# Performance work log

Measured on AMD Instinct MI355X. Metric: run time of the kernel, lower is better.

The kernel has to match this reference:

```python
import jax, jax.numpy as jnp
import numpy as np
import math

B, S, H = 8, 160, 768
DEP = 64
NH, DH = 12, H // 12
W_EDGE = 1.0
EPS = 1e-5


def setup_inputs() -> dict:
    key = jax.random.key(0)
    ks = jax.random.split(key, 16)
    sc_h = 1.0 / math.sqrt(H)
    sc_d = 1.0 / math.sqrt(DEP)
    return {
        "token_feature": jax.random.normal(ks[0], (B, S, H), jnp.float32),
        "edge_feature": jax.random.normal(ks[1], (B, S, S, DEP), jnp.float32),
        "dependency_masks": jax.random.randint(ks[2], (B, S, S), 0, 2, jnp.int32),
        "Wq": jax.random.normal(ks[3], (H, H), jnp.float32) * sc_h,
        "bq": jnp.zeros((H,), jnp.float32),
        "Wk": jax.random.normal(ks[4], (H, H), jnp.float32) * sc_h,
        "bk": jnp.zeros((H,), jnp.float32),
        "Wv": jax.random.normal(ks[5], (H, H), jnp.float32) * sc_h,
        "bv": jnp.zeros((H,), jnp.float32),
        "Wek": jax.random.normal(ks[6], (DEP, H), jnp.float32) * sc_d,
        "bek": jnp.zeros((H,), jnp.float32),
        "Wev": jax.random.normal(ks[7], (DEP, H), jnp.float32) * sc_d,
        "bev": jnp.zeros((H,), jnp.float32),
        "ln_g": jnp.ones((H,), jnp.float32),
        "ln_b": jnp.zeros((H,), jnp.float32),
    }


def _heads3(x):  # [B,S,H] -> [B,NH,S,DH]
    return x.reshape(B, S, NH, DH).transpose(0, 2, 1, 3)


def _heads4(x):  # [B,S,S,H] -> [B,NH,S,S,DH]
    return x.reshape(B, S, S, NH, DH).transpose(0, 3, 1, 2, 4)


def reference(token_feature, edge_feature, dependency_masks,
              Wq, bq, Wk, bk, Wv, bv, Wek, bek, Wev, bev, ln_g, ln_b):
    q = _heads3(token_feature @ Wq + bq)   # [B,NH,S,DH]
    k = _heads3(token_feature @ Wk + bk)
    v = _heads3(token_feature @ Wv + bv)
    ek = _heads4(edge_feature @ Wek + bek)  # [B,NH,S,S,DH]
    ev = _heads4(edge_feature @ Wev + bev)
    # key_ij = k_j + w*ek_ij ; scores_ij = q_i . key_ij / sqrt(dh)
    scores = (jnp.einsum('bhid,bhjd->bhij', q, k)
              + W_EDGE * jnp.einsum('bhid,bhijd->bhij', q, ek))
    scores = scores / math.sqrt(DH)
    mask = (dependency_masks[:, None, :, :] == 0)  # [B,1,S,S]
    scores = jnp.where(mask, jnp.float32(-10000.0), scores)
    probs = jax.nn.softmax(scores, axis=-1)  # dropout is identity in eval
    ctx = (jnp.einsum('bhij,bhjd->bhid', probs, v)
           + W_EDGE * jnp.einsum('bhij,bhijd->bhid', probs, ev))
    ctx = ctx.transpose(0, 2, 1, 3).reshape(B, S, H)
    x = token_feature + ctx
    mu = jnp.mean(x, axis=-1, keepdims=True)
    var = jnp.mean(jnp.square(x - mu), axis=-1, keepdims=True)
    return (x - mu) / jnp.sqrt(var + EPS) * ln_g + ln_b
```

## Files before the change

### kernel.cpp

```cpp
#include <hip/hip_runtime.h>
#include <hip/hip_bf16.h>
#include <math.h>

#define BB 8
#define SS 160
#define HH 768
#define DEPTH 64
#define NHEAD 12
#define DHEAD 64
#define BS (BB*SS)

constexpr float EPS_C = 1e-5f;

typedef __attribute__((ext_vector_type(8))) short bf16x8;
typedef __attribute__((ext_vector_type(4))) float f32x4;

__device__ inline short f2bs(float x) {
    union { __hip_bfloat16 b; short s; } u;
    u.b = __float2bfloat16(x);
    return u.s;
}

__global__ __launch_bounds__(256) void cast_x(
    const float* __restrict__ X, __hip_bfloat16* __restrict__ Xb)
{
    int idx = blockIdx.x * 256 + threadIdx.x;
    float4 xin = ((const float4*)X)[idx];
    __hip_bfloat16* o = Xb + (size_t)idx * 4;
    o[0] = __float2bfloat16(xin.x); o[1] = __float2bfloat16(xin.y);
    o[2] = __float2bfloat16(xin.z); o[3] = __float2bfloat16(xin.w);
}

__global__ __launch_bounds__(256) void transpose_cast_w(
    const float* __restrict__ Wq, const float* __restrict__ Wk,
    const float* __restrict__ Wv, __hip_bfloat16* __restrict__ WT)
{
    __shared__ float t[32][33];
    const float* W = (blockIdx.z == 0) ? Wq : (blockIdx.z == 1) ? Wk : Wv;
    __hip_bfloat16* o = WT + (size_t)blockIdx.z * HH * HH;
    int kt = blockIdx.x * 32, nt = blockIdx.y * 32;
    int tx = threadIdx.x & 31, ty = threadIdx.x >> 5;
#pragma unroll
    for (int r = 0; r < 32; r += 8)
        t[ty + r][tx] = W[(size_t)(kt + ty + r) * HH + nt + tx];
    __syncthreads();
#pragma unroll
    for (int r = 0; r < 32; r += 8)
        o[(size_t)(nt + ty + r) * HH + kt + tx] = __float2bfloat16(t[tx][ty + r]);
}

__global__ __launch_bounds__(256) void gemm_qkv(
    const __hip_bfloat16* __restrict__ Xb, const __hip_bfloat16* __restrict__ WT,
    const float* __restrict__ bq, const float* __restrict__ bk,
    const float* __restrict__ bv,
    __hip_bfloat16* __restrict__ qb, __hip_bfloat16* __restrict__ kb,
    __hip_bfloat16* __restrict__ vb)
{
    __shared__ int4 sA[4][128];
    __shared__ int4 sB[4][64];
    int m0 = blockIdx.x * 128, n0 = blockIdx.y * 64, mat = blockIdx.z;
    const short* X = (const short*)Xb;
    const short* W = (const short*)WT + (size_t)mat * HH * HH;
    const float* bias = (mat == 0) ? bq : (mat == 1) ? bk : bv;
    int tid = threadIdx.x, w = tid >> 6, l = tid & 63;
    int wm = (w >> 1) * 64, wn = (w & 1) * 32;
    int khalf = l >> 4, lc = l & 15;

    f32x4 acc[4][2];
#pragma unroll
    for (int i = 0; i < 4; i++)
#pragma unroll
        for (int j = 0; j < 2; j++) acc[i][j] = (f32x4){0.f, 0.f, 0.f, 0.f};

    for (int k0 = 0; k0 < HH; k0 += 32) {
        __syncthreads();
        sA[w][l]      = *(const int4*)(X + (size_t)(m0 + l) * HH + k0 + w * 8);
        sA[w][l + 64] = *(const int4*)(X + (size_t)(m0 + l + 64) * HH + k0 + w * 8);
        sB[w][l]      = *(const int4*)(W + (size_t)(n0 + l) * HH + k0 + w * 8);
        __syncthreads();
        bf16x8 b0 = *(const bf16x8*)&sB[khalf][wn + lc];
        bf16x8 b1 = *(const bf16x8*)&sB[khalf][wn + 16 + lc];
#pragma unroll
        for (int mi = 0; mi < 4; mi++) {
            bf16x8 a = *(const bf16x8*)&sA[khalf][wm + mi * 16 + lc];
            acc[mi][0] = __builtin_amdgcn_mfma_f32_16x16x32_bf16(a, b0, acc[mi][0], 0, 0, 0);
            acc[mi][1] = __builtin_amdgcn_mfma_f32_16x16x32_bf16(a, b1, acc[mi][1], 0, 0, 0);
        }
    }

    int rg = (l >> 4) * 4;
    __hip_bfloat16* outm = (mat == 0) ? qb : (mat == 1) ? kb : vb;
#pragma unroll
    for (int ni = 0; ni < 2; ni++) {
        int gcol = n0 + wn + ni * 16 + lc;
        float bv_ = bias[gcol];
#pragma unroll
        for (int mi = 0; mi < 4; mi++) {
            int grow = m0 + wm + mi * 16 + rg;
            f32x4 a = acc[mi][ni];
            __hip_bfloat16* o = outm + (size_t)grow * HH + gcol;
            o[0]      = __float2bfloat16(a.x + bv_);
            o[HH]     = __float2bfloat16(a.y + bv_);
            o[2 * HH] = __float2bfloat16(a.z + bv_);
            o[3 * HH] = __float2bfloat16(a.w + bv_);
        }
    }
}

__global__ __launch_bounds__(256) void scores_gemm(
    const __hip_bfloat16* __restrict__ qb, const __hip_bfloat16* __restrict__ kb,
    _Float16* __restrict__ sc)
{
    __shared__ int4 sQ[8][160];
    __shared__ int4 sK[8][160];
    int h = blockIdx.x, b = blockIdx.y;
    const short* Q = (const short*)qb + (size_t)b * SS * HH + h * DHEAD;
    const short* K = (const short*)kb + (size_t)b * SS * HH + h * DHEAD;
    int tid = threadIdx.x, w = tid >> 6, l = tid & 63;

    for (int idx = tid; idx < SS * 8; idx += 256) {
        int row = idx >> 3, ch = idx & 7;
        sQ[ch][row] = *(const int4*)(Q + (size_t)row * HH + ch * 8);
        sK[ch][row] = *(const int4*)(K + (size_t)row * HH + ch * 8);
    }
    __syncthreads();

    int wm = (w >> 1) * 80, wn = (w & 1) * 80;
    int khalf = l >> 4, lc = l & 15;
    f32x4 acc[5][5];
#pragma unroll
    for (int i = 0; i < 5; i++)
#pragma unroll
        for (int j = 0; j < 5; j++) acc[i][j] = (f32x4){0.f, 0.f, 0.f, 0.f};

#pragma unroll
    for (int s = 0; s < 2; s++) {
        int c = s * 4 + khalf;
        bf16x8 bf[5];
#pragma unroll
        for (int ni = 0; ni < 5; ni++)
            bf[ni] = *(const bf16x8*)&sK[c][wn + ni * 16 + lc];
#pragma unroll
        for (int mi = 0; mi < 5; mi++) {
            bf16x8 a = *(const bf16x8*)&sQ[c][wm + mi * 16 + lc];
#pragma unroll
            for (int ni = 0; ni < 5; ni++)
                acc[mi][ni] = __builtin_amdgcn_mfma_f32_16x16x32_bf16(a, bf[ni], acc[mi][ni], 0, 0, 0);
        }
    }

    int rg = (l >> 4) * 4;
    _Float16* base = sc + (size_t)(b * NHEAD + h) * SS * SS;
#pragma unroll
    for (int mi = 0; mi < 5; mi++) {
        int i0 = wm + mi * 16 + rg;
#pragma unroll
        for (int ni = 0; ni < 5; ni++) {
            int j = wn + ni * 16 + lc;
            f32x4 a = acc[mi][ni];
            base[(size_t)(i0 + 0) * SS + j] = (_Float16)(a.x * 0.125f);
            base[(size_t)(i0 + 1) * SS + j] = (_Float16)(a.y * 0.125f);
            base[(size_t)(i0 + 2) * SS + j] = (_Float16)(a.z * 0.125f);
            base[(size_t)(i0 + 3) * SS + j] = (_Float16)(a.w * 0.125f);
        }
    }
}

__global__ __launch_bounds__(256) void qek_gemm(
    const __hip_bfloat16* __restrict__ qb, const float* __restrict__ Wek,
    __hip_bfloat16* __restrict__ qek)
{
    int task = blockIdx.x * 4 + (threadIdx.x >> 6);
    int l = threadIdx.x & 63;
    int mt = task / NHEAD, h = task - mt * NHEAD;
    int bi0 = mt * 16;
    int lr = l & 15, kg = l >> 4;
    const short* Q = (const short*)qb;

    bf16x8 a0 = *(const bf16x8*)(Q + (size_t)(bi0 + lr) * HH + h * DHEAD + kg * 8);
    bf16x8 a1 = *(const bf16x8*)(Q + (size_t)(bi0 + lr) * HH + h * DHEAD + 32 + kg * 8);

    short* O = (short*)qek;
#pragma unroll
    for (int nt = 0; nt < 4; nt++) {
        int d = nt * 16 + lr;
        const float* wp = Wek + (size_t)d * HH + h * DHEAD + kg * 8;
        float4 w0 = *(const float4*)(wp);
        float4 w1 = *(const float4*)(wp + 4);
        float4 w2 = *(const float4*)(wp + 32);
        float4 w3 = *(const float4*)(wp + 36);
        bf16x8 b0, b1;
        b0[0]=f2bs(w0.x); b0[1]=f2bs(w0.y); b0[2]=f2bs(w0.z); b0[3]=f2bs(w0.w);
        b0[4]=f2bs(w1.x); b0[5]=f2bs(w1.y); b0[6]=f2bs(w1.z); b0[7]=f2bs(w1.w);
        b1[0]=f2bs(w2.x); b1[1]=f2bs(w2.y); b1[2]=f2bs(w2.z); b1[3]=f2bs(w2.w);
        b1[4]=f2bs(w3.x); b1[5]=f2bs(w3.y); b1[6]=f2bs(w3.z); b1[7]=f2bs(w3.w);
        f32x4 acc = (f32x4){0.f, 0.f, 0.f, 0.f};
        acc = __builtin_amdgcn_mfma_f32_16x16x32_bf16(a0, b0, acc, 0, 0, 0);
        acc = __builtin_amdgcn_mfma_f32_16x16x32_bf16(a1, b1, acc, 0, 0, 0);
        int row0 = bi0 + kg * 4;
#pragma unroll
        for (int r = 0; r < 4; r++)
            O[(size_t)(row0 + r) * HH + h * DHEAD + nt * 16 + lr] = f2bs(acc[r]);
    }
}

__global__ __launch_bounds__(256) void escore_add(
    const float* __restrict__ edge, const __hip_bfloat16* __restrict__ qek,
    _Float16* __restrict__ sc)
{
    int bi = blockIdx.x * 4 + (threadIdx.x >> 6);
    int l = threadIdx.x & 63;
    int b = bi / SS, i = bi - b * SS;
    int lr = l & 15, kg = l >> 4;
    const short* QE = (const short*)qek + (size_t)bi * HH;

    bf16x8 qe0 = *(const bf16x8*)(QE + lr * DHEAD + kg * 8);
    bf16x8 qe1 = *(const bf16x8*)(QE + lr * DHEAD + 32 + kg * 8);

    const float* E = edge + (size_t)bi * SS * DEPTH;
    int h = lr, hc = (h < NHEAD) ? h : (NHEAD - 1);
    bool hvalid = (h < NHEAD);
    _Float16* srow = sc + ((size_t)(b * NHEAD + hc) * SS + i) * SS;

#pragma unroll 2
    for (int jt = 0; jt < 10; jt++) {
        const float* ep = E + (size_t)(jt * 16 + lr) * DEPTH + kg * 8;
        float4 e0 = *(const float4*)(ep);
        float4 e1 = *(const float4*)(ep + 4);
        float4 e2 = *(const float4*)(ep + 32);
        float4 e3 = *(const float4*)(ep + 36);
        bf16x8 a0, a1;
        a0[0]=f2bs(e0.x); a0[1]=f2bs(e0.y); a0[2]=f2bs(e0.z); a0[3]=f2bs(e0.w);
        a0[4]=f2bs(e1.x); a0[5]=f2bs(e1.y); a0[6]=f2bs(e1.z); a0[7]=f2bs(e1.w);
        a1[0]=f2bs(e2.x); a1[1]=f2bs(e2.y); a1[2]=f2bs(e2.z); a1[3]=f2bs(e2.w);
        a1[4]=f2bs(e3.x); a1[5]=f2bs(e3.y); a1[6]=f2bs(e3.z); a1[7]=f2bs(e3.w);
        f32x4 acc = (f32x4){0.f, 0.f, 0.f, 0.f};
        acc = __builtin_amdgcn_mfma_f32_16x16x32_bf16(a0, qe0, acc, 0, 0, 0);
        acc = __builtin_amdgcn_mfma_f32_16x16x32_bf16(a1, qe1, acc, 0, 0, 0);
        if (hvalid) {
            int j0 = jt * 16 + kg * 4;
            _Float16* p = srow + j0;
            p[0] = (_Float16)((float)p[0] + 0.125f * acc[0]);
            p[1] = (_Float16)((float)p[1] + 0.125f * acc[1]);
            p[2] = (_Float16)((float)p[2] + 0.125f * acc[2]);
            p[3] = (_Float16)((float)p[3] + 0.125f * acc[3]);
        }
    }
}

__global__ __launch_bounds__(256) void attn_kernel(
    const float* __restrict__ token, const float* __restrict__ edge,
    const int* __restrict__ mask,
    const __hip_bfloat16* __restrict__ q_ws, const _Float16* __restrict__ sc,
    const __hip_bfloat16* __restrict__ v_ws,
    const float* __restrict__ bek,
    const float* __restrict__ Wev, const float* __restrict__ bev,
    const float* __restrict__ ln_g, const float* __restrict__ ln_b,
    float* __restrict__ out)
{
    __shared__ float  s_q[HH];
    __shared__ float  s_scores[NHEAD][SS];
    __shared__ float  s_pe[NHEAD][DEPTH];
    __shared__ float  s_x[HH];
    __shared__ float  s_qbek[NHEAD];
    __shared__ int    s_mask[SS];
    __shared__ float  s_red[8];

    int bi = blockIdx.x;
    int b  = bi / SS;
    int i  = bi - b * SS;
    int tid = threadIdx.x;
    int w = tid >> 6, l = tid & 63;

    for (int c = tid; c < HH; c += 256)
        s_q[c] = __bfloat162float(q_ws[(size_t)bi * HH + c]);
    if (tid < SS) s_mask[tid] = mask[(size_t)bi * SS + tid];
    __syncthreads();

    if (tid < NHEAD) {
        const float* qp = s_q + tid * DHEAD;
        const float* bp = bek + tid * DHEAD;
        float sum = 0.f;
#pragma unroll
        for (int c = 0; c < DHEAD; c++) sum += qp[c] * bp[c];
        s_qbek[tid] = sum;
    }
    __syncthreads();

    const _Float16* scp = sc + (size_t)(b * NHEAD) * (SS * SS) + (size_t)i * SS;
    for (int idx = tid; idx < NHEAD * SS; idx += 256) {
        int h = idx / SS, j = idx - h * SS;
        float qk = (float)scp[(size_t)h * (SS * SS) + j];
        s_scores[h][j] = s_mask[j] ? (qk + 0.125f * s_qbek[h]) : -10000.0f;
    }
    __syncthreads();

    for (int h = w; h < NHEAD; h += 4) {
        float v0 = s_scores[h][l];
        float v1 = s_scores[h][l + 64];
        float v2 = (l < 32) ? s_scores[h][l + 128] : -INFINITY;
        float mx = fmaxf(v0, fmaxf(v1, v2));
#pragma unroll
        for (int mm = 32; mm >= 1; mm >>= 1) mx = fmaxf(mx, __shfl_xor(mx, mm, 64));
        float e0 = expf(v0 - mx), e1 = expf(v1 - mx);
        float e2 = (l < 32) ? expf(v2 - mx) : 0.f;
        float sm = e0 + e1 + e2;
#pragma unroll
        for (int mm = 32; mm >= 1; mm >>= 1) sm += __shfl_xor(sm, mm, 64);
        float inv = 1.0f / sm;
        s_scores[h][l]      = e0 * inv;
        s_scores[h][l + 64] = e1 * inv;
        if (l < 32) s_scores[h][l + 128] = e2 * inv;
    }
    __syncthreads();

    const float* e_row = edge + (size_t)bi * SS * DEPTH;
    {
        int h0 = w * 3;
        float av0 = 0.f, av1 = 0.f, av2 = 0.f;
        float pe0 = 0.f, pe1 = 0.f, pe2 = 0.f;
        const __hip_bfloat16* vbp = v_ws + (size_t)b * SS * HH + h0 * DHEAD + l;
        const float* er = e_row + l;
        const float* p0r = &s_scores[h0][0];
        const float* p1r = &s_scores[h0 + 1][0];
        const float* p2r = &s_scores[h0 + 2][0];
#pragma unroll 4
        for (int j = 0; j < SS; j++) {
            float p0 = p0r[j], p1 = p1r[j], p2 = p2r[j];
            const __hip_bfloat16* vp = vbp + (size_t)j * HH;
            av0 += p0 * __bfloat162float(vp[0]);
            av1 += p1 * __bfloat162float(vp[DHEAD]);
            av2 += p2 * __bfloat162float(vp[2 * DHEAD]);
            float ev = er[(size_t)j * DEPTH];
            pe0 += p0 * ev; pe1 += p1 * ev; pe2 += p2 * ev;
        }
        s_pe[h0][l]     = pe0;
        s_pe[h0 + 1][l] = pe1;
        s_pe[h0 + 2][l] = pe2;
        s_q[h0 * DHEAD + l]       = av0;
        s_q[(h0 + 1) * DHEAD + l] = av1;
        s_q[(h0 + 2) * DHEAD + l] = av2;
    }
    __syncthreads();

    for (int mdx = tid; mdx < HH; mdx += 256) {
        int h = mdx >> 6;
        const float* pep = &s_pe[h][0];
        float sum = 0.f;
#pragma unroll
        for (int d = 0; d < DEPTH; d++) sum += pep[d] * Wev[(size_t)d * HH + mdx];
        float ctx = s_q[mdx] + (sum + bev[mdx]);
        s_x[mdx] = token[(size_t)bi * HH + mdx] + ctx;
    }
    __syncthreads();

    float lsum = 0.f, lsq = 0.f;
    for (int c = tid; c < HH; c += 256) {
        float x = s_x[c];
        lsum += x; lsq += x * x;
    }
#pragma unroll
    for (int mm = 32; mm >= 1; mm >>= 1) {
        lsum += __shfl_xor(lsum, mm, 64);
        lsq  += __shfl_xor(lsq,  mm, 64);
    }
    if (l == 0) { s_red[w] = lsum; s_red[4 + w] = lsq; }
    __syncthreads();
    float tsum = s_red[0] + s_red[1] + s_red[2] + s_red[3];
    float tsq  = s_red[4] + s_red[5] + s_red[6] + s_red[7];
    float mu  = tsum / HH;
    float var = tsq / HH - mu * mu;
    float rstd = rsqrtf(var + EPS_C);
    for (int c = tid; c < HH; c += 256)
        out[(size_t)bi * HH + c] = (s_x[c] - mu) * rstd * ln_g[c] + ln_b[c];
}

extern "C" void kernel_launch(void* const* d_in, const int* in_sizes, int n_in,
                              void* d_out, int out_size, void* d_ws, size_t ws_size,
                              hipStream_t stream) {
    const float* token = (const float*)d_in[0];
    const float* edge  = (const float*)d_in[1];
    const int*   mask  = (const int*)d_in[2];
    const float* Wq = (const float*)d_in[3];  const float* bq = (const float*)d_in[4];
    const float* Wk = (const float*)d_in[5];  const float* bk = (const float*)d_in[6];
    const float* Wv = (const float*)d_in[7];  const float* bv = (const float*)d_in[8];
    const float* Wek = (const float*)d_in[9];  const float* bek = (const float*)d_in[10];
    const float* Wev = (const float*)d_in[11]; const float* bev = (const float*)d_in[12];
    const float* ln_g = (const float*)d_in[13]; const float* ln_b = (const float*)d_in[14];
    float* out = (float*)d_out;

    __hip_bfloat16* qb = (__hip_bfloat16*)d_ws;
    __hip_bfloat16* kb = qb + (size_t)BS * HH;
    __hip_bfloat16* vb = kb + (size_t)BS * HH;
    __hip_bfloat16* Xb = vb + (size_t)BS * HH;
    __hip_bfloat16* WT = Xb + (size_t)BS * HH;
    _Float16*       sc = (_Float16*)Xb;
    __hip_bfloat16* qek = kb;

    cast_x<<<(BS * HH / 4) / 256, 256, 0, stream>>>(token, Xb);
    transpose_cast_w<<<dim3(24, 24, 3), 256, 0, stream>>>(Wq, Wk, Wv, WT);
    gemm_qkv<<<dim3(BS / 128, HH / 64, 3), 256, 0, stream>>>(
        Xb, WT, bq, bk, bv, qb, kb, vb);
    scores_gemm<<<dim3(NHEAD, BB), 256, 0, stream>>>(qb, kb, sc);
    qek_gemm<<<240, 256, 0, stream>>>(qb, Wek, qek);
    escore_add<<<BS / 4, 256, 0, stream>>>(edge, qek, sc);
    attn_kernel<<<BS, 256, 0, stream>>>(token, edge, mask, qb, sc, vb,
                                        bek, Wev, bev, ln_g, ln_b, out);
}
```

Before: 108.9 us.

## Fuse edge-score MFMA into attention kernel and restructure qek GEMM with shared weights

Removes the separate escore_add kernel and computes the q·ek edge scores inside attn_kernel, adding them straight into the shared-memory score rows. This drops the fp16 read-modify-write of the score tensor and lets the edge row loaded for the edge-score step be reused later in the same block. The qek GEMM is rewritten to stage Wek once per head in LDS and reuse it across several row tiles. The q·bek dot product now uses a shuffle reduction, and the PV loop handles two keys per iteration. One fewer launch, but attn_kernel takes on more MFMA work and register pressure.

```diff
diff --git a/kernel.cpp b/kernel.cpp
--- a/kernel.cpp
+++ b/kernel.cpp
@@ -19,6 +19,11 @@
     union { __hip_bfloat16 b; short s; } u;
     u.b = __float2bfloat16(x);
     return u.s;
+}
+__device__ inline float bs2f(short s) {
+    union { short s; __hip_bfloat16 b; } u;
+    u.s = s;
+    return __bfloat162float(u.b);
 }
 
 __global__ __launch_bounds__(256) void cast_x(
@@ -166,84 +171,55 @@
     }
 }
 
-__global__ __launch_bounds__(256) void qek_gemm(
+__global__ __launch_bounds__(256) void qek_slim(
     const __hip_bfloat16* __restrict__ qb, const float* __restrict__ Wek,
     __hip_bfloat16* __restrict__ qek)
 {
-    int task = blockIdx.x * 4 + (threadIdx.x >> 6);
-    int l = threadIdx.x & 63;
-    int mt = task / NHEAD, h = task - mt * NHEAD;
-    int bi0 = mt * 16;
+    __shared__ short sW[8 * 65 * 8];
+    int h = blockIdx.x, mg = blockIdx.y;
+    int tid = threadIdx.x, w = tid >> 6, l = tid & 63;
     int lr = l & 15, kg = l >> 4;
-    const short* Q = (const short*)qb;
-
-    bf16x8 a0 = *(const bf16x8*)(Q + (size_t)(bi0 + lr) * HH + h * DHEAD + kg * 8);
-    bf16x8 a1 = *(const bf16x8*)(Q + (size_t)(bi0 + lr) * HH + h * DHEAD + 32 + kg * 8);
-
-    short* O = (short*)qek;
-#pragma unroll
-    for (int nt = 0; nt < 4; nt++) {
-        int d = nt * 16 + lr;
-        const float* wp = Wek + (size_t)d * HH + h * DHEAD + kg * 8;
+
+    {
+        int d = tid >> 2, q4 = tid & 3;
+        const float* wp = Wek + (size_t)d * HH + h * DHEAD + q4 * 16;
         float4 w0 = *(const float4*)(wp);
         float4 w1 = *(const float4*)(wp + 4);
-        float4 w2 = *(const float4*)(wp + 32);
-        float4 w3 = *(const float4*)(wp + 36);
-        bf16x8 b0, b1;
-        b0[0]=f2bs(w0.x); b0[1]=f2bs(w0.y); b0[2]=f2bs(w0.z); b0[3]=f2bs(w0.w);
-        b0[4]=f2bs(w1.x); b0[5]=f2bs(w1.y); b0[6]=f2bs(w1.z); b0[7]=f2bs(w1.w);
-        b1[0]=f2bs(w2.x); b1[1]=f2bs(w2.y); b1[2]=f2bs(w2.z); b1[3]=f2bs(w2.w);
-        b1[4]=f2bs(w3.x); b1[5]=f2bs(w3.y); b1[6]=f2bs(w3.z); b1[7]=f2bs(w3.w);
-        f32x4 acc = (f32x4){0.f, 0.f, 0.f, 0.f};
-        acc = __builtin_amdgcn_mfma_f32_16x16x32_bf16(a0, b0, acc, 0, 0, 0);
-        acc = __builtin_amdgcn_mfma_f32_16x16x32_bf16(a1, b1, acc, 0, 0, 0);
-        int row0 = bi0 + kg * 4;
-#pragma unroll
-        for (int r = 0; r < 4; r++)
-            O[(size_t)(row0 + r) * HH + h * DHEAD + nt * 16 + lr] = f2bs(acc[r]);
-    }
-}
-
-__global__ __launch_bounds__(256) void escore_add(
-    const float* __restrict__ edge, const __hip_bfloat16* __restrict__ qek,
-    _Float16* __restrict__ sc)
-{
-    int bi = blockIdx.x * 4 + (threadIdx.x >> 6);
-    int l = threadIdx.x & 63;
-    int b = bi / SS, i = bi - b * SS;
-    int lr = l & 15, kg = l >> 4;
-    const short* QE = (const short*)qek + (size_t)bi * HH;
-
-    bf16x8 qe0 = *(const bf16x8*)(QE + lr * DHEAD + kg * 8);
-    bf16x8 qe1 = *(const bf16x8*)(QE + lr * DHEAD + 32 + kg * 8);
-
-    const float* E = edge + (size_t)bi * SS * DEPTH;
-    int h = lr, hc = (h < NHEAD) ? h : (NHEAD - 1);
-    bool hvalid = (h < NHEAD);
-    _Float16* srow = sc + ((size_t)(b * NHEAD + hc) * SS + i) * SS;
-
-#pragma unroll 2
-    for (int jt = 0; jt < 10; jt++) {
-        const float* ep = E + (size_t)(jt * 16 + lr) * DEPTH + kg * 8;
-        float4 e0 = *(const float4*)(ep);
-        float4 e1 = *(const float4*)(ep + 4);
-        float4 e2 = *(const float4*)(ep + 32);
-        float4 e3 = *(const float4*)(ep + 36);
-        bf16x8 a0, a1;
-        a0[0]=f2bs(e0.x); a0[1]=f2bs(e0.y); a0[2]=f2bs(e0.z); a0[3]=f2bs(e0.w);
-        a0[4]=f2bs(e1.x); a0[5]=f2bs(e1.y); a0[6]=f2bs(e1.z); a0[7]=f2bs(e1.w);
-        a1[0]=f2bs(e2.x); a1[1]=f2bs(e2.y); a1[2]=f2bs(e2.z); a1[3]=f2bs(e2.w);
-        a1[4]=f2bs(e3.x); a1[5]=f2bs(e3.y); a1[6]=f2bs(e3.z); a1[7]=f2bs(e3.w);
-        f32x4 acc = (f32x4){0.f, 0.f, 0.f, 0.f};
-        acc = __builtin_amdgcn_mfma_f32_16x16x32_bf16(a0, qe0, acc, 0, 0, 0);
-        acc = __builtin_amdgcn_mfma_f32_16x16x32_bf16(a1, qe1, acc, 0, 0, 0);
-        if (hvalid) {
-            int j0 = jt * 16 + kg * 4;
-            _Float16* p = srow + j0;
-            p[0] = (_Float16)((float)p[0] + 0.125f * acc[0]);
-            p[1] = (_Float16)((float)p[1] + 0.125f * acc[1]);
-            p[2] = (_Float16)((float)p[2] + 0.125f * acc[2]);
-            p[3] = (_Float16)((float)p[3] + 0.125f * acc[3]);
+        float4 w2 = *(const float4*)(wp + 8);
+        float4 w3 = *(const float4*)(wp + 12);
+        bf16x8 p0, p1;
+        p0[0]=f2bs(w0.x); p0[1]=f2bs(w0.y); p0[2]=f2bs(w0.z); p0[3]=f2bs(w0.w);
+        p0[4]=f2bs(w1.x); p0[5]=f2bs(w1.y); p0[6]=f2bs(w1.z); p0[7]=f2bs(w1.w);
+        p1[0]=f2bs(w2.x); p1[1]=f2bs(w2.y); p1[2]=f2bs(w2.z); p1[3]=f2bs(w2.w);
+        p1[4]=f2bs(w3.x); p1[5]=f2bs(w3.y); p1[6]=f2bs(w3.z); p1[7]=f2bs(w3.w);
+        *(bf16x8*)&sW[((q4 * 2) * 65 + d) * 8]     = p0;
+        *(bf16x8*)&sW[((q4 * 2 + 1) * 65 + d) * 8] = p1;
+    }
+    __syncthreads();
+
+    bf16x8 bfrag[2][4];
+#pragma unroll
+    for (int s = 0; s < 2; s++)
+#pragma unroll
+        for (int nt = 0; nt < 4; nt++)
+            bfrag[s][nt] = *(const bf16x8*)&sW[((s * 4 + kg) * 65 + nt * 16 + lr) * 8];
+
+    const short* Q = (const short*)qb;
+    short* O = (short*)qek;
+#pragma unroll
+    for (int mi = 0; mi < 2; mi++) {
+        int m0 = (mg * 8 + w * 2 + mi) * 16;
+        bf16x8 a0 = *(const bf16x8*)(Q + (size_t)(m0 + lr) * HH + h * DHEAD + kg * 8);
+        bf16x8 a1 = *(const bf16x8*)(Q + (size_t)(m0 + lr) * HH + h * DHEAD + 32 + kg * 8);
+#pragma unroll
+        for (int nt = 0; nt < 4; nt++) {
+            f32x4 acc = (f32x4){0.f, 0.f, 0.f, 0.f};
+            acc = __builtin_amdgcn_mfma_f32_16x16x32_bf16(a0, bfrag[0][nt], acc, 0, 0, 0);
+            acc = __builtin_amdgcn_mfma_f32_16x16x32_bf16(a1, bfrag[1][nt], acc, 0, 0, 0);
+            int row0 = m0 + kg * 4;
+#pragma unroll
+            for (int r = 0; r < 4; r++)
+                O[(size_t)(row0 + r) * HH + h * DHEAD + nt * 16 + lr] = f2bs(acc[r]);
         }
     }
 }
@@ -252,13 +228,13 @@
     const float* __restrict__ token, const float* __restrict__ edge,
     const int* __restrict__ mask,
     const __hip_bfloat16* __restrict__ q_ws, const _Float16* __restrict__ sc,
-    const __hip_bfloat16* __restrict__ v_ws,
+    const __hip_bfloat16* __restrict__ v_ws, const __hip_bfloat16* __restrict__ qek,
     const float* __restrict__ bek,
     const float* __restrict__ Wev, const float* __restrict__ bev,
     const float* __restrict__ ln_g, const float* __restrict__ ln_b,
     float* __restrict__ out)
 {
-    __shared__ float  s_q[HH];
+    __shared__ float  s_ctx[HH];
     __shared__ float  s_scores[NHEAD][SS];
     __shared__ float  s_pe[NHEAD][DEPTH];
     __shared__ float  s_x[HH];
@@ -271,19 +247,24 @@
     int i  = bi - b * SS;
     int tid = threadIdx.x;
     int w = tid >> 6, l = tid & 63;
-
-    for (int c = tid; c < HH; c += 256)
-        s_q[c] = __bfloat162float(q_ws[(size_t)bi * HH + c]);
+    int lr = l & 15, kg = l >> 4;
+
     if (tid < SS) s_mask[tid] = mask[(size_t)bi * SS + tid];
-    __syncthreads();
-
-    if (tid < NHEAD) {
-        const float* qp = s_q + tid * DHEAD;
-        const float* bp = bek + tid * DHEAD;
-        float sum = 0.f;
-#pragma unroll
-        for (int c = 0; c < DHEAD; c++) sum += qp[c] * bp[c];
-        s_qbek[tid] = sum;
+
+    {
+        int hs = w * 3 + kg;
+        float part = 0.f;
+        if (hs < NHEAD) {
+            const __hip_bfloat16* qp = q_ws + (size_t)bi * HH + hs * DHEAD + lr * 4;
+            float4 bv4 = *(const float4*)(bek + hs * DHEAD + lr * 4);
+            part = __bfloat162float(qp[0]) * bv4.x + __bfloat162float(qp[1]) * bv4.y
+                 + __bfloat162float(qp[2]) * bv4.z + __bfloat162float(qp[3]) * bv4.w;
+        }
+        part += __shfl_xor(part, 1, 64);
+        part += __shfl_xor(part, 2, 64);
+        part += __shfl_xor(part, 4, 64);
+        part += __shfl_xor(part, 8, 64);
+        if (lr == 0 && hs < NHEAD) s_qbek[hs] = part;
     }
     __syncthreads();
 
@@ -295,6 +276,36 @@
     }
     __syncthreads();
 
+    const float* e_row = edge + (size_t)bi * SS * DEPTH;
+    {
+        const short* QE = (const short*)qek + (size_t)bi * HH;
+        bf16x8 qe0 = *(const bf16x8*)(QE + lr * DHEAD + kg * 8);
+        bf16x8 qe1 = *(const bf16x8*)(QE + lr * DHEAD + 32 + kg * 8);
+        for (int jt = w; jt < 10; jt += 4) {
+            const float* ep = e_row + (size_t)(jt * 16 + lr) * DEPTH + kg * 8;
+            float4 e0 = *(const float4*)(ep);
+            float4 e1 = *(const float4*)(ep + 4);
+            float4 e2 = *(const float4*)(ep + 32);
+            float4 e3 = *(const float4*)(ep + 36);
+            bf16x8 a0, a1;
+            a0[0]=f2bs(e0.x); a0[1]=f2bs(e0.y); a0[2]=f2bs(e0.z); a0[3]=f2bs(e0.w);
+            a0[4]=f2bs(e1.x); a0[5]=f2bs(e1.y); a0[6]=f2bs(e1.z); a0[7]=f2bs(e1.w);
+            a1[0]=f2bs(e2.x); a1[1]=f2bs(e2.y); a1[2]=f2bs(e2.z); a1[3]=f2bs(e2.w);
+            a1[4]=f2bs(e3.x); a1[5]=f2bs(e3.y); a1[6]=f2bs(e3.z); a1[7]=f2bs(e3.w);
+            f32x4 acc = (f32x4){0.f, 0.f, 0.f, 0.f};
+            acc = __builtin_amdgcn_mfma_f32_16x16x32_bf16(a0, qe0, acc, 0, 0, 0);
+            acc = __builtin_amdgcn_mfma_f32_16x16x32_bf16(a1, qe1, acc, 0, 0, 0);
+            if (lr < NHEAD) {
+                int j0 = jt * 16 + kg * 4;
+#pragma unroll
+                for (int r = 0; r < 4; r++)
+                    if (s_mask[j0 + r])
+                        s_scores[lr][j0 + r] += 0.125f * acc[r];
+            }
+        }
+    }
+    __syncthreads();
+
     for (int h = w; h < NHEAD; h += 4) {
         float v0 = s_scores[h][l];
         float v1 = s_scores[h][l + 64];
@@ -314,32 +325,36 @@
     }
     __syncthreads();
 
-    const float* e_row = edge + (size_t)bi * SS * DEPTH;
     {
         int h0 = w * 3;
         float av0 = 0.f, av1 = 0.f, av2 = 0.f;
         float pe0 = 0.f, pe1 = 0.f, pe2 = 0.f;
         const __hip_bfloat16* vbp = v_ws + (size_t)b * SS * HH + h0 * DHEAD + l;
         const float* er = e_row + l;
-        const float* p0r = &s_scores[h0][0];
-        const float* p1r = &s_scores[h0 + 1][0];
-        const float* p2r = &s_scores[h0 + 2][0];
-#pragma unroll 4
-        for (int j = 0; j < SS; j++) {
-            float p0 = p0r[j], p1 = p1r[j], p2 = p2r[j];
-            const __hip_bfloat16* vp = vbp + (size_t)j * HH;
-            av0 += p0 * __bfloat162float(vp[0]);
-            av1 += p1 * __bfloat162float(vp[DHEAD]);
-            av2 += p2 * __bfloat162float(vp[2 * DHEAD]);
-            float ev = er[(size_t)j * DEPTH];
-            pe0 += p0 * ev; pe1 += p1 * ev; pe2 += p2 * ev;
+#pragma unroll 2
+        for (int j0 = 0; j0 < SS; j0 += 2) {
+            float2 p0 = *(const float2*)(&s_scores[h0][j0]);
+            float2 p1 = *(const float2*)(&s_scores[h0 + 1][j0]);
+            float2 p2 = *(const float2*)(&s_scores[h0 + 2][j0]);
+            const __hip_bfloat16* vp = vbp + (size_t)j0 * HH;
+            av0 += p0.x * __bfloat162float(vp[0])
+                 + p0.y * __bfloat162float(vp[HH]);
+            av1 += p1.x * __bfloat162float(vp[DHEAD])
+                 + p1.y * __bfloat162float(vp[HH + DHEAD]);
+            av2 += p2.x * __bfloat162float(vp[2 * DHEAD])
+                 + p2.y * __bfloat162float(vp[HH + 2 * DHEAD]);
+            float ev0 = er[(size_t)j0 * DEPTH];
+            float ev1 = er[(size_t)(j0 + 1) * DEPTH];
+            pe0 += p0.x * ev0 + p0.y * ev1;
+            pe1 += p1.x * ev0 + p1.y * ev1;
+            pe2 += p2.x * ev0 + p2.y * ev1;
         }
         s_pe[h0][l]     = pe0;
         s_pe[h0 + 1][l] = pe1;
         s_pe[h0 + 2][l] = pe2;
-        s_q[h0 * DHEAD + l]       = av0;
-        s_q[(h0 + 1) * DHEAD + l] = av1;
-        s_q[(h0 + 2) * DHEAD + l] = av2;
+        s_ctx[h0 * DHEAD + l]       = av0;
+        s_ctx[(h0 + 1) * DHEAD + l] = av1;
+        s_ctx[(h0 + 2) * DHEAD + l] = av2;
     }
     __syncthreads();
 
@@ -349,7 +364,7 @@
         float sum = 0.f;
 #pragma unroll
         for (int d = 0; d < DEPTH; d++) sum += pep[d] * Wev[(size_t)d * HH + mdx];
-        float ctx = s_q[mdx] + (sum + bev[mdx]);
+        float ctx = s_ctx[mdx] + (sum + bev[mdx]);
         s_x[mdx] = token[(size_t)bi * HH + mdx] + ctx;
     }
     __syncthreads();
@@ -402,8 +417,7 @@
     gemm_qkv<<<dim3(BS / 128, HH / 64, 3), 256, 0, stream>>>(
         Xb, WT, bq, bk, bv, qb, kb, vb);
     scores_gemm<<<dim3(NHEAD, BB), 256, 0, stream>>>(qb, kb, sc);
-    qek_gemm<<<240, 256, 0, stream>>>(qb, Wek, qek);
-    escore_add<<<BS / 4, 256, 0, stream>>>(edge, qek, sc);
-    attn_kernel<<<BS, 256, 0, stream>>>(token, edge, mask, qb, sc, vb,
+    qek_slim<<<dim3(NHEAD, 10), 256, 0, stream>>>(qb, Wek, qek);
+    attn_kernel<<<BS, 256, 0, stream>>>(token, edge, mask, qb, sc, vb, qek,
                                         bek, Wev, bev, ln_g, ln_b, out);
 }
```

New measurement: 111.3 us. 2.2% more time.
